# Performance work log

Measured on AMD Instinct MI355X. Metric: run time of the kernel, lower is better.

The kernel has to match this reference:

```python
import jax, jax.numpy as jnp
import numpy as np

D_MODEL = 1024
D_FF = 2048        # SwiGLU hidden (first linear outputs 2*D_FF)
NUM_EXPERTS = 8
TOP_K = 2
BATCH, SEQ = 2, 2048


def setup_inputs() -> dict:
    key = jax.random.key(0)
    ks = jax.random.split(key, 5)
    s = 0.02
    x = jax.random.normal(ks[0], (BATCH, SEQ, D_MODEL), jnp.float32)
    Wr = jax.random.normal(ks[1], (D_MODEL, NUM_EXPERTS), jnp.float32) * s
    temp = jnp.ones((1,), jnp.float32)  # router_temp parameter
    W1 = jax.random.normal(ks[2], (NUM_EXPERTS, D_MODEL, 2 * D_FF), jnp.float32) * s
    b1 = jnp.zeros((NUM_EXPERTS, 2 * D_FF), jnp.float32)
    W2 = jax.random.normal(ks[3], (NUM_EXPERTS, D_FF, D_MODEL), jnp.float32) * s
    b2 = jnp.zeros((NUM_EXPERTS, D_MODEL), jnp.float32)
    return {"x": x, "Wr": Wr, "temp": temp, "W1": W1, "b1": b1, "W2": W2, "b2": b2}


def reference(x, Wr, temp, W1, b1, W2, b2):
    # Eval-mode forward: no router noise, dropout is identity.
    B, S, D = x.shape
    xf = x.reshape(-1, D)                       # [T, D], T = B*S
    logits = (xf @ Wr) / temp                   # [T, E]
    topw, topi = jax.lax.top_k(logits, TOP_K)   # [T, K]
    topw = jax.nn.softmax(topw, axis=-1)        # renormalized top-k weights
    out = jnp.zeros_like(xf)
    for e in range(NUM_EXPERTS):                # small fixed expert count
        h = xf @ W1[e] + b1[e]                  # [T, 2F]
        a, g = jnp.split(h, 2, axis=-1)         # SwiGLU: a * silu(g)
        y = (a * jax.nn.silu(g)) @ W2[e] + b2[e]  # [T, D]
        # combine weight for expert e (0 if not routed to e)
        we = jnp.sum(jnp.where(topi == e, topw, 0.0), axis=-1, keepdims=True)
        out = out + y * we
    return out.reshape(B, S, D)
```

## Files before the change

kernel.cpp:

```cpp
#include <hip/hip_runtime.h>
#include <hip/hip_bf16.h>
#include <math.h>


#define T_TOK  4096
#define DMODEL 1024
#define NEXP   8
#define FF     2048
#define FF2    4096

typedef __bf16 bf16_t;
typedef bf16_t bf16x8 __attribute__((ext_vector_type(8)));
typedef float  f32x4  __attribute__((ext_vector_type(4)));

__device__ __forceinline__ void gload_lds16(const void* g, void* l) {
  __builtin_amdgcn_global_load_lds((const __attribute__((address_space(1))) void*)g,
                                   (__attribute__((address_space(3))) void*)l, 16, 0, 0);
}

__global__ __launch_bounds__(256) void moe_router(
    const float* __restrict__ x, const float* __restrict__ Wr,
    const float* __restrict__ temp,
    bf16_t* __restrict__ xb,
    int* __restrict__ cnt, int* __restrict__ tok_list, float* __restrict__ w_list,
    int* __restrict__ slot)
{
  __shared__ float sWr[DMODEL * NEXP];
  for (int i = threadIdx.x; i < DMODEL * NEXP; i += 256) sWr[i] = Wr[i];
  __syncthreads();

  int wave = threadIdx.x >> 6, lane = threadIdx.x & 63;
  int t = blockIdx.x * 4 + wave;
  const float* xr = x + (size_t)t * DMODEL;

  f32x4 acc0 = {0.f, 0.f, 0.f, 0.f}, acc1 = {0.f, 0.f, 0.f, 0.f};
  #pragma unroll
  for (int i = 0; i < 16; ++i) {
    int d = lane + 64 * i;
    float v = xr[d];
    xb[(size_t)t * DMODEL + d] = (bf16_t)v;
    const f32x4* wr = (const f32x4*)&sWr[d * NEXP];
    acc0 += v * wr[0];
    acc1 += v * wr[1];
  }
  #pragma unroll
  for (int off = 32; off; off >>= 1) {
    #pragma unroll
    for (int q = 0; q < 4; ++q) {
      acc0[q] += __shfl_down(acc0[q], off, 64);
      acc1[q] += __shfl_down(acc1[q], off, 64);
    }
  }
  if (lane == 0) {
    float invt = 1.f / temp[0];
    float lg[NEXP] = {acc0[0], acc0[1], acc0[2], acc0[3],
                      acc1[0], acc1[1], acc1[2], acc1[3]};
    int bi = 0, si = 0;
    float best = -3.4e38f, sec = -3.4e38f;
    #pragma unroll
    for (int e = 0; e < NEXP; ++e) {
      float l = lg[e] * invt;
      if (l > best)     { sec = best; si = bi; best = l; bi = e; }
      else if (l > sec) { sec = l; si = e; }
    }
    float ex = expf(sec - best);
    float wb  = 1.f / (1.f + ex);
    float wsc = ex  / (1.f + ex);
    int p0 = atomicAdd(&cnt[bi], 1);
    tok_list[bi * T_TOK + p0] = t; w_list[bi * T_TOK + p0] = wb;
    int p1 = atomicAdd(&cnt[si], 1);
    tok_list[si * T_TOK + p1] = t; w_list[si * T_TOK + p1] = wsc;
    slot[2 * t]     = bi * T_TOK + p0;
    slot[2 * t + 1] = si * T_TOK + p1;
  }
}

__global__ void moe_prefix(const int* __restrict__ cnt, int* __restrict__ offs) {
  if (threadIdx.x == 0) {
    int s = 0;
    for (int e = 0; e < NEXP; ++e) { offs[e] = s; s += cnt[e]; }
    offs[NEXP] = s;
  }
}

__global__ __launch_bounds__(256) void tcast_fast(
    const float* __restrict__ in, bf16_t* __restrict__ outp, int R, int C)
{
  __shared__ float tile[64][65];
  const float* inp = in + (size_t)blockIdx.z * R * C;
  bf16_t* op = outp + (size_t)blockIdx.z * R * C;
  int c0 = blockIdx.x * 64, r0 = blockIdx.y * 64;
  int tid = threadIdx.x;
  int lr = tid >> 4;
  int lc4 = (tid & 15) * 4;
  #pragma unroll
  for (int p = 0; p < 4; ++p) {
    int r = p * 16 + lr;
    const float4 v = *(const float4*)&inp[(size_t)(r0 + r) * C + c0 + lc4];
    tile[r][lc4 + 0] = v.x; tile[r][lc4 + 1] = v.y;
    tile[r][lc4 + 2] = v.z; tile[r][lc4 + 3] = v.w;
  }
  __syncthreads();
  int rr8 = (tid & 7) * 8;
  #pragma unroll
  for (int it = 0; it < 2; ++it) {
    int cc = (tid >> 3) + it * 32;
    bf16x8 o;
    #pragma unroll
    for (int j = 0; j < 8; ++j) o[j] = (bf16_t)tile[rr8 + j][cc];
    *(bf16x8*)&op[(size_t)(c0 + cc) * R + r0 + rr8] = o;
  }
}

__global__ __launch_bounds__(256) void moe_gemm1(
    const bf16_t* __restrict__ xb, const bf16_t* __restrict__ W1t,
    const float* __restrict__ b1, const int* __restrict__ cnt,
    const int* __restrict__ offs, const int* __restrict__ tok_list,
    const float* __restrict__ w_list, bf16_t* __restrict__ U,
    int e_base, long estride)
{
  int e = e_base + blockIdx.z;
  int count = cnt[e];
  int m0 = blockIdx.y * 128;
  if (m0 >= count) return;
  int nt = blockIdx.x;
  const bf16_t* W1e = W1t + (size_t)blockIdx.z * estride;

  __shared__ bf16_t As[128 * 64];
  __shared__ bf16_t Bs[128 * 64];
  __shared__ int   stok[128];
  __shared__ float sw[128];
  int tid = threadIdx.x;
  if (tid < 128) {
    int m = m0 + tid;
    stok[tid] = (m < count) ? tok_list[e * T_TOK + m] : 0;
    sw[tid]   = (m < count) ? w_list[e * T_TOK + m] : 0.f;
  }
  __syncthreads();

  int wave = tid >> 6, lane = tid & 63;
  int quad = lane >> 4, l16 = lane & 15;
  int rsub = lane >> 3;
  int swz  = (lane & 7) ^ rsub;

  size_t asrc[4]; const bf16_t* bsrc[4];
  bf16_t* aldst[4]; bf16_t* bldst[4];
  #pragma unroll
  for (int s = 0; s < 4; ++s) {
    int inst = wave * 4 + s;
    int row = inst * 8 + rsub;
    asrc[s] = (size_t)stok[row] * DMODEL + swz * 8;
    int grow = (row < 64) ? (nt * 64 + row) : (FF + nt * 64 + (row - 64));
    bsrc[s] = W1e + (size_t)grow * DMODEL + swz * 8;
    aldst[s] = As + inst * 512;
    bldst[s] = Bs + inst * 512;
  }

  f32x4 acc[2][8];
  #pragma unroll
  for (int i = 0; i < 2; ++i)
    #pragma unroll
    for (int j = 0; j < 8; ++j) acc[i][j] = (f32x4){0.f, 0.f, 0.f, 0.f};

  for (int k0 = 0; k0 < DMODEL; k0 += 64) {
    __syncthreads();
    #pragma unroll
    for (int s = 0; s < 4; ++s) {
      gload_lds16(xb + asrc[s] + k0, aldst[s]);
      gload_lds16(bsrc[s] + k0, bldst[s]);
    }
    __syncthreads();
    #pragma unroll
    for (int kh = 0; kh < 2; ++kh) {
      int so = ((kh * 4 + quad) ^ (l16 & 7)) * 8;
      bf16x8 a0 = *(const bf16x8*)&As[(wave * 32      + l16) * 64 + so];
      bf16x8 a1 = *(const bf16x8*)&As[(wave * 32 + 16 + l16) * 64 + so];
      #pragma unroll
      for (int j = 0; j < 8; ++j) {
        bf16x8 b = *(const bf16x8*)&Bs[(j * 16 + l16) * 64 + so];
        acc[0][j] = __builtin_amdgcn_mfma_f32_16x16x32_bf16(a0, b, acc[0][j], 0, 0, 0);
        acc[1][j] = __builtin_amdgcn_mfma_f32_16x16x32_bf16(a1, b, acc[1][j], 0, 0, 0);
      }
    }
  }

  int uoff = offs[e];
  const float* b1e = b1 + (size_t)e * FF2;
  #pragma unroll
  for (int j = 0; j < 4; ++j) {
    int f = nt * 64 + j * 16 + l16;
    float ba = b1e[f];
    float bg = b1e[FF + f];
    #pragma unroll
    for (int i = 0; i < 2; ++i) {
      f32x4 av = acc[i][j];
      f32x4 gv = acc[i][j + 4];
      #pragma unroll
      for (int r = 0; r < 4; ++r) {
        int m = wave * 32 + i * 16 + quad * 4 + r;
        if (m0 + m < count) {
          float aa = av[r] + ba;
          float gg = gv[r] + bg;
          float u = sw[m] * aa * gg / (1.f + __expf(-gg));
          U[(size_t)(uoff + m0 + m) * FF + f] = (bf16_t)u;
        }
      }
    }
  }
}

__global__ __launch_bounds__(256) void moe_gemm2(
    const bf16_t* __restrict__ U, const bf16_t* __restrict__ W2t,
    const int* __restrict__ cnt, const int* __restrict__ offs,
    float* __restrict__ Y,
    int e_base, long estride)
{
  int e = e_base + blockIdx.z;
  int count = cnt[e];
  int m0 = blockIdx.y * 128;
  if (m0 >= count) return;
  int n0 = blockIdx.x * 128;
  const bf16_t* W2e = W2t + (size_t)blockIdx.z * estride;

  __shared__ bf16_t As[128 * 64];
  __shared__ bf16_t Bs[128 * 64];
  int tid = threadIdx.x;
  int wave = tid >> 6, lane = tid & 63;
  int quad = lane >> 4, l16 = lane & 15;
  int rsub = lane >> 3;
  int swz  = (lane & 7) ^ rsub;
  int uoff = offs[e];

  const bf16_t* asrc[4]; const bf16_t* bsrc[4];
  bf16_t* aldst[4]; bf16_t* bldst[4];
  #pragma unroll
  for (int s = 0; s < 4; ++s) {
    int inst = wave * 4 + s;
    int row = inst * 8 + rsub;
    asrc[s] = U   + (size_t)(uoff + m0 + row) * FF + swz * 8;
    bsrc[s] = W2e + (size_t)(n0 + row)        * FF + swz * 8;
    aldst[s] = As + inst * 512;
    bldst[s] = Bs + inst * 512;
  }

  f32x4 acc[2][8];
  #pragma unroll
  for (int i = 0; i < 2; ++i)
    #pragma unroll
    for (int j = 0; j < 8; ++j) acc[i][j] = (f32x4){0.f, 0.f, 0.f, 0.f};

  for (int k0 = 0; k0 < FF; k0 += 64) {
    __syncthreads();
    #pragma unroll
    for (int s = 0; s < 4; ++s) {
      gload_lds16(asrc[s] + k0, aldst[s]);
      gload_lds16(bsrc[s] + k0, bldst[s]);
    }
    __syncthreads();
    #pragma unroll
    for (int kh = 0; kh < 2; ++kh) {
      int so = ((kh * 4 + quad) ^ (l16 & 7)) * 8;
      bf16x8 a0 = *(const bf16x8*)&As[(wave * 32      + l16) * 64 + so];
      bf16x8 a1 = *(const bf16x8*)&As[(wave * 32 + 16 + l16) * 64 + so];
      #pragma unroll
      for (int j = 0; j < 8; ++j) {
        bf16x8 b = *(const bf16x8*)&Bs[(j * 16 + l16) * 64 + so];
        acc[0][j] = __builtin_amdgcn_mfma_f32_16x16x32_bf16(a0, b, acc[0][j], 0, 0, 0);
        acc[1][j] = __builtin_amdgcn_mfma_f32_16x16x32_bf16(a1, b, acc[1][j], 0, 0, 0);
      }
    }
  }

  #pragma unroll
  for (int j = 0; j < 8; ++j) {
    int n = n0 + j * 16 + l16;
    #pragma unroll
    for (int i = 0; i < 2; ++i) {
      f32x4 av = acc[i][j];
      #pragma unroll
      for (int r = 0; r < 4; ++r) {
        int m = wave * 32 + i * 16 + quad * 4 + r;
        if (m0 + m < count)
          Y[(size_t)(uoff + m0 + m) * DMODEL + n] = av[r];
      }
    }
  }
}

__global__ __launch_bounds__(256) void moe_combine(
    const float* __restrict__ Y, const float* __restrict__ b2,
    const int* __restrict__ slot, const float* __restrict__ w_list,
    const int* __restrict__ offs, float* __restrict__ out)
{
  int t = blockIdx.x;
  int v0 = slot[2 * t], v1 = slot[2 * t + 1];
  int e0 = v0 >> 12, p0 = v0 & (T_TOK - 1);
  int e1 = v1 >> 12, p1 = v1 & (T_TOK - 1);
  int r0 = offs[e0] + p0, r1 = offs[e1] + p1;
  float w0 = w_list[v0], w1 = w_list[v1];
  int d = threadIdx.x * 4;
  f32x4 y0 = *(const f32x4*)&Y[(size_t)r0 * DMODEL + d];
  f32x4 y1 = *(const f32x4*)&Y[(size_t)r1 * DMODEL + d];
  f32x4 c0 = *(const f32x4*)&b2[(size_t)e0 * DMODEL + d];
  f32x4 c1 = *(const f32x4*)&b2[(size_t)e1 * DMODEL + d];
  *(f32x4*)&out[(size_t)t * DMODEL + d] = y0 + y1 + w0 * c0 + w1 * c1;
}

extern "C" void kernel_launch(void* const* d_in, const int* in_sizes, int n_in,
                              void* d_out, int out_size, void* d_ws, size_t ws_size,
                              hipStream_t stream)
{
  const float* x    = (const float*)d_in[0];
  const float* Wr   = (const float*)d_in[1];
  const float* temp = (const float*)d_in[2];
  const float* W1   = (const float*)d_in[3];
  const float* b1   = (const float*)d_in[4];
  const float* W2   = (const float*)d_in[5];
  const float* b2   = (const float*)d_in[6];
  float* out = (float*)d_out;

  char* ws = (char*)d_ws;
  size_t off = 0;
  auto alloc = [&](size_t b) { void* p = ws + off; off += (b + 255) & ~(size_t)255; return p; };
  bf16_t* xb  = (bf16_t*)alloc((size_t)T_TOK * DMODEL * 2);
  bf16_t* U   = (bf16_t*)alloc((size_t)(2 * T_TOK + 128) * FF * 2);
  float*  Y   = (float*)alloc((size_t)(2 * T_TOK) * DMODEL * 4);
  int*   cnt  = (int*)alloc(256);
  int*   offs = (int*)alloc(256);
  int*   tok  = (int*)alloc((size_t)NEXP * T_TOK * 4);
  float* wl   = (float*)alloc((size_t)NEXP * T_TOK * 4);
  int*   slot = (int*)alloc((size_t)2 * T_TOK * 4);
  size_t base = off;
  const size_t W1T_FULL = (size_t)NEXP * FF2 * DMODEL * 2;
  const size_t W2T_FULL = (size_t)NEXP * DMODEL * FF * 2;
  bool batched = (ws_size >= base + W1T_FULL + W2T_FULL);

  hipMemsetAsync(cnt, 0, NEXP * sizeof(int), stream);
  moe_router<<<dim3(T_TOK / 4), dim3(256), 0, stream>>>(x, Wr, temp, xb, cnt, tok, wl, slot);
  moe_prefix<<<dim3(1), dim3(64), 0, stream>>>(cnt, offs);

  if (batched) {
    bf16_t* W1t = (bf16_t*)alloc(W1T_FULL);
    bf16_t* W2t = (bf16_t*)alloc(W2T_FULL);
    tcast_fast<<<dim3(FF2 / 64, DMODEL / 64, NEXP), dim3(256), 0, stream>>>(W1, W1t, DMODEL, FF2);
    tcast_fast<<<dim3(DMODEL / 64, FF / 64, NEXP), dim3(256), 0, stream>>>(W2, W2t, FF, DMODEL);
    moe_gemm1<<<dim3(FF / 64, T_TOK / 128, NEXP), dim3(256), 0, stream>>>(
        xb, W1t, b1, cnt, offs, tok, wl, U, 0, (long)FF2 * DMODEL);
    moe_gemm2<<<dim3(DMODEL / 128, T_TOK / 128, NEXP), dim3(256), 0, stream>>>(
        U, W2t, cnt, offs, Y, 0, (long)DMODEL * FF);
  } else {
    bf16_t* W1t = (bf16_t*)alloc((size_t)FF2 * DMODEL * 2);
    bf16_t* W2t = (bf16_t*)alloc((size_t)DMODEL * FF * 2);
    for (int e = 0; e < NEXP; ++e) {
      tcast_fast<<<dim3(FF2 / 64, DMODEL / 64, 1), dim3(256), 0, stream>>>(
          W1 + (size_t)e * DMODEL * FF2, W1t, DMODEL, FF2);
      moe_gemm1<<<dim3(FF / 64, T_TOK / 128, 1), dim3(256), 0, stream>>>(
          xb, W1t, b1, cnt, offs, tok, wl, U, e, 0);
    }
    for (int e = 0; e < NEXP; ++e) {
      tcast_fast<<<dim3(DMODEL / 64, FF / 64, 1), dim3(256), 0, stream>>>(
          W2 + (size_t)e * FF * DMODEL, W2t, FF, DMODEL);
      moe_gemm2<<<dim3(DMODEL / 128, T_TOK / 128, 1), dim3(256), 0, stream>>>(
          U, W2t, cnt, offs, Y, e, 0);
    }
  }
  moe_combine<<<dim3(T_TOK), dim3(256), 0, stream>>>(Y, b2, slot, wl, offs, out);
}
```

Before: 536.5 us.

## Rewrite gemm1 as 256x256 double-buffered pipelined tile with 8 waves

The first expert GEMM moves from a 128x128 single-buffered tile with 4 waves to a 256x(128 up + 128 gate) tile with 8 waves and 2 blocks per CU. LDS is double-buffered, and global-to-LDS loads for the next K step are interleaved between four MFMA phases, with s_setprio raised around the MFMA bursts. The aim is to hide load latency behind compute and raise arithmetic intensity per LDS byte. In exchange it uses far more LDS and registers, and padding waste grows for experts whose token counts are not multiples of 256.

```diff
diff --git a/kernel.cpp b/kernel.cpp
--- a/kernel.cpp
+++ b/kernel.cpp
@@ -8,6 +8,7 @@
 #define NEXP   8
 #define FF     2048
 #define FF2    4096
+#define NT1    16
 
 typedef __bf16 bf16_t;
 typedef bf16_t bf16x8 __attribute__((ext_vector_type(8)));
@@ -17,6 +18,10 @@
   __builtin_amdgcn_global_load_lds((const __attribute__((address_space(1))) void*)g,
                                    (__attribute__((address_space(3))) void*)l, 16, 0, 0);
 }
+
+#define BARF() do { asm volatile("" ::: "memory"); \
+                    __builtin_amdgcn_s_barrier();  \
+                    asm volatile("" ::: "memory"); } while (0)
 
 __global__ __launch_bounds__(256) void moe_router(
     const float* __restrict__ x, const float* __restrict__ Wr,
@@ -112,7 +117,18 @@
   }
 }
 
-__global__ __launch_bounds__(256) void moe_gemm1(
+#define STG_A1(buf, ha, kk) do { \
+    gload_lds16(xb + asrc[ha][0] + (kk), &As[buf][aofs[ha][0]]); \
+    gload_lds16(xb + asrc[ha][1] + (kk), &As[buf][aofs[ha][1]]); } while (0)
+#define STG_B1(buf, hb, kk) do { \
+    gload_lds16(W1e + bsrc[hb][0] + (kk), &Bs[buf][bofs[hb][0]]); \
+    gload_lds16(W1e + bsrc[hb][1] + (kk), &Bs[buf][bofs[hb][1]]); } while (0)
+#define LDA1(dst, rowbase, kh_) \
+    dst = *(const bf16x8*)&As[cur][((rowbase) + l16) * 64 + ((((kh_) * 4 + quad) ^ (l16 & 7)) * 8)]
+#define LDB1(dst, rowbase, kh_) \
+    dst = *(const bf16x8*)&Bs[cur][((rowbase) + l16) * 64 + ((((kh_) * 4 + quad) ^ (l16 & 7)) * 8)]
+
+__global__ __launch_bounds__(512, 2) void moe_gemm1(
     const bf16_t* __restrict__ xb, const bf16_t* __restrict__ W1t,
     const float* __restrict__ b1, const int* __restrict__ cnt,
     const int* __restrict__ offs, const int* __restrict__ tok_list,
@@ -121,92 +137,152 @@
 {
   int e = e_base + blockIdx.z;
   int count = cnt[e];
-  int m0 = blockIdx.y * 128;
+  int m0 = blockIdx.y * 256;
   if (m0 >= count) return;
   int nt = blockIdx.x;
   const bf16_t* W1e = W1t + (size_t)blockIdx.z * estride;
 
-  __shared__ bf16_t As[128 * 64];
-  __shared__ bf16_t Bs[128 * 64];
-  __shared__ int   stok[128];
-  __shared__ float sw[128];
+  __shared__ bf16_t As[2][256 * 64];
+  __shared__ bf16_t Bs[2][256 * 64];
+
   int tid = threadIdx.x;
-  if (tid < 128) {
-    int m = m0 + tid;
-    stok[tid] = (m < count) ? tok_list[e * T_TOK + m] : 0;
-    sw[tid]   = (m < count) ? w_list[e * T_TOK + m] : 0.f;
-  }
-  __syncthreads();
-
-  int wave = tid >> 6, lane = tid & 63;
+  int w = tid >> 6, lane = tid & 63;
+  int wm = w >> 2, wn = w & 3;
   int quad = lane >> 4, l16 = lane & 15;
-  int rsub = lane >> 3;
-  int swz  = (lane & 7) ^ rsub;
-
-  size_t asrc[4]; const bf16_t* bsrc[4];
-  bf16_t* aldst[4]; bf16_t* bldst[4];
-  #pragma unroll
-  for (int s = 0; s < 4; ++s) {
-    int inst = wave * 4 + s;
-    int row = inst * 8 + rsub;
-    asrc[s] = (size_t)stok[row] * DMODEL + swz * 8;
-    int grow = (row < 64) ? (nt * 64 + row) : (FF + nt * 64 + (row - 64));
-    bsrc[s] = W1e + (size_t)grow * DMODEL + swz * 8;
-    aldst[s] = As + inst * 512;
-    bldst[s] = Bs + inst * 512;
-  }
-
-  f32x4 acc[2][8];
-  #pragma unroll
-  for (int i = 0; i < 2; ++i)
-    #pragma unroll
-    for (int j = 0; j < 8; ++j) acc[i][j] = (f32x4){0.f, 0.f, 0.f, 0.f};
-
-  for (int k0 = 0; k0 < DMODEL; k0 += 64) {
-    __syncthreads();
-    #pragma unroll
-    for (int s = 0; s < 4; ++s) {
-      gload_lds16(xb + asrc[s] + k0, aldst[s]);
-      gload_lds16(bsrc[s] + k0, bldst[s]);
-    }
-    __syncthreads();
-    #pragma unroll
-    for (int kh = 0; kh < 2; ++kh) {
-      int so = ((kh * 4 + quad) ^ (l16 & 7)) * 8;
-      bf16x8 a0 = *(const bf16x8*)&As[(wave * 32      + l16) * 64 + so];
-      bf16x8 a1 = *(const bf16x8*)&As[(wave * 32 + 16 + l16) * 64 + so];
-      #pragma unroll
-      for (int j = 0; j < 8; ++j) {
-        bf16x8 b = *(const bf16x8*)&Bs[(j * 16 + l16) * 64 + so];
-        acc[0][j] = __builtin_amdgcn_mfma_f32_16x16x32_bf16(a0, b, acc[0][j], 0, 0, 0);
-        acc[1][j] = __builtin_amdgcn_mfma_f32_16x16x32_bf16(a1, b, acc[1][j], 0, 0, 0);
-      }
-    }
+  int rsub = lane >> 3, csub = lane & 7;
+  int swz = csub ^ rsub;
+
+  unsigned asrc[2][2], bsrc[2][2];
+  int aofs[2][2], bofs[2][2];
+  #pragma unroll
+  for (int h = 0; h < 2; ++h) {
+    #pragma unroll
+    for (int i = 0; i < 2; ++i) {
+      int rb = h * 128 + w * 16 + i * 8;
+      int r = rb + rsub;
+      int gm = m0 + r;
+      int tokr = (gm < count) ? tok_list[e * T_TOK + gm] : 0;
+      asrc[h][i] = (unsigned)tokr * DMODEL + swz * 8;
+      aofs[h][i] = rb * 64;
+      int wn_r = r >> 6, j = r & 63;
+      int f = nt * 128 + wn_r * 32 + (j & 31);
+      bsrc[h][i] = (unsigned)((j < 32) ? f : (FF + f)) * DMODEL + swz * 8;
+      bofs[h][i] = rb * 64;
+    }
+  }
+
+  f32x4 acc[8][4];
+  #pragma unroll
+  for (int m = 0; m < 8; ++m)
+    #pragma unroll
+    for (int n = 0; n < 4; ++n) acc[m][n] = (f32x4){0.f, 0.f, 0.f, 0.f};
+  bf16x8 a0[4][2], a1[4][2], bb[2][2];
+
+  STG_A1(0, 0, 0); STG_A1(0, 1, 0);
+  STG_B1(0, 0, 0); STG_B1(0, 1, 0);
+  STG_A1(1, 0, 64); STG_A1(1, 1, 64);
+  asm volatile("s_waitcnt vmcnt(4)" ::: "memory");
+  BARF();
+
+  for (int t = 0; t < NT1; ++t) {
+    const int cur = t & 1, nxt = cur ^ 1;
+    const int k1 = ((t + 1 < NT1) ? t + 1 : NT1 - 1) * 64;
+    const int k2 = ((t + 2 < NT1) ? t + 2 : NT1 - 1) * 64;
+
+    STG_B1(nxt, 0, k1);
+    #pragma unroll
+    for (int m = 0; m < 4; ++m)
+      #pragma unroll
+      for (int kh = 0; kh < 2; ++kh) LDA1(a0[m][kh], wm * 128 + m * 16, kh);
+    #pragma unroll
+    for (int n = 0; n < 2; ++n)
+      #pragma unroll
+      for (int kh = 0; kh < 2; ++kh) LDB1(bb[n][kh], wn * 64 + n * 16, kh);
+    BARF();
+    __builtin_amdgcn_s_setprio(1);
+    #pragma unroll
+    for (int m = 0; m < 4; ++m)
+      #pragma unroll
+      for (int n = 0; n < 2; ++n)
+        #pragma unroll
+        for (int kh = 0; kh < 2; ++kh)
+          acc[m][n] = __builtin_amdgcn_mfma_f32_16x16x32_bf16(a0[m][kh], bb[n][kh], acc[m][n], 0, 0, 0);
+    __builtin_amdgcn_s_setprio(0);
+    BARF();
+
+    STG_B1(nxt, 1, k1);
+    #pragma unroll
+    for (int m = 0; m < 4; ++m)
+      #pragma unroll
+      for (int kh = 0; kh < 2; ++kh) LDA1(a1[m][kh], wm * 128 + 64 + m * 16, kh);
+    BARF();
+    __builtin_amdgcn_s_setprio(1);
+    #pragma unroll
+    for (int m = 0; m < 4; ++m)
+      #pragma unroll
+      for (int n = 0; n < 2; ++n)
+        #pragma unroll
+        for (int kh = 0; kh < 2; ++kh)
+          acc[4 + m][n] = __builtin_amdgcn_mfma_f32_16x16x32_bf16(a1[m][kh], bb[n][kh], acc[4 + m][n], 0, 0, 0);
+    __builtin_amdgcn_s_setprio(0);
+    BARF();
+
+    STG_A1(cur, 0, k2);
+    #pragma unroll
+    for (int n = 0; n < 2; ++n)
+      #pragma unroll
+      for (int kh = 0; kh < 2; ++kh) LDB1(bb[n][kh], wn * 64 + (2 + n) * 16, kh);
+    BARF();
+    __builtin_amdgcn_s_setprio(1);
+    #pragma unroll
+    for (int m = 0; m < 4; ++m)
+      #pragma unroll
+      for (int n = 0; n < 2; ++n)
+        #pragma unroll
+        for (int kh = 0; kh < 2; ++kh)
+          acc[m][2 + n] = __builtin_amdgcn_mfma_f32_16x16x32_bf16(a0[m][kh], bb[n][kh], acc[m][2 + n], 0, 0, 0);
+    __builtin_amdgcn_s_setprio(0);
+    BARF();
+
+    STG_A1(cur, 1, k2);
+    __builtin_amdgcn_s_setprio(1);
+    #pragma unroll
+    for (int m = 0; m < 4; ++m)
+      #pragma unroll
+      for (int n = 0; n < 2; ++n)
+        #pragma unroll
+        for (int kh = 0; kh < 2; ++kh)
+          acc[4 + m][2 + n] = __builtin_amdgcn_mfma_f32_16x16x32_bf16(a1[m][kh], bb[n][kh], acc[4 + m][2 + n], 0, 0, 0);
+    __builtin_amdgcn_s_setprio(0);
+    asm volatile("s_waitcnt vmcnt(4)" ::: "memory");
+    BARF();
   }
 
   int uoff = offs[e];
   const float* b1e = b1 + (size_t)e * FF2;
   #pragma unroll
-  for (int j = 0; j < 4; ++j) {
-    int f = nt * 64 + j * 16 + l16;
+  for (int nf = 0; nf < 2; ++nf) {
+    int f = nt * 128 + wn * 32 + nf * 16 + l16;
     float ba = b1e[f];
     float bg = b1e[FF + f];
     #pragma unroll
-    for (int i = 0; i < 2; ++i) {
-      f32x4 av = acc[i][j];
-      f32x4 gv = acc[i][j + 4];
+    for (int m = 0; m < 8; ++m) {
+      f32x4 av = acc[m][nf];
+      f32x4 gv = acc[m][2 + nf];
       #pragma unroll
       for (int r = 0; r < 4; ++r) {
-        int m = wave * 32 + i * 16 + quad * 4 + r;
-        if (m0 + m < count) {
+        int row = wm * 128 + m * 16 + quad * 4 + r;
+        if (m0 + row < count) {
+          float wv = w_list[e * T_TOK + m0 + row];
           float aa = av[r] + ba;
           float gg = gv[r] + bg;
-          float u = sw[m] * aa * gg / (1.f + __expf(-gg));
-          U[(size_t)(uoff + m0 + m) * FF + f] = (bf16_t)u;
+          float u = wv * aa * gg / (1.f + __expf(-gg));
+          U[(size_t)(uoff + m0 + row) * FF + f] = (bf16_t)u;
         }
       }
     }
   }
+  asm volatile("s_waitcnt vmcnt(0)" ::: "memory");
 }
 
 __global__ __launch_bounds__(256) void moe_gemm2(
@@ -344,7 +420,7 @@
     bf16_t* W2t = (bf16_t*)alloc(W2T_FULL);
     tcast_fast<<<dim3(FF2 / 64, DMODEL / 64, NEXP), dim3(256), 0, stream>>>(W1, W1t, DMODEL, FF2);
     tcast_fast<<<dim3(DMODEL / 64, FF / 64, NEXP), dim3(256), 0, stream>>>(W2, W2t, FF, DMODEL);
-    moe_gemm1<<<dim3(FF / 64, T_TOK / 128, NEXP), dim3(256), 0, stream>>>(
+    moe_gemm1<<<dim3(FF / 128, T_TOK / 256, NEXP), dim3(512), 0, stream>>>(
         xb, W1t, b1, cnt, offs, tok, wl, U, 0, (long)FF2 * DMODEL);
     moe_gemm2<<<dim3(DMODEL / 128, T_TOK / 128, NEXP), dim3(256), 0, stream>>>(
         U, W2t, cnt, offs, Y, 0, (long)DMODEL * FF);
@@ -354,7 +430,7 @@
     for (int e = 0; e < NEXP; ++e) {
       tcast_fast<<<dim3(FF2 / 64, DMODEL / 64, 1), dim3(256), 0, stream>>>(
           W1 + (size_t)e * DMODEL * FF2, W1t, DMODEL, FF2);
-      moe_gemm1<<<dim3(FF / 64, T_TOK / 128, 1), dim3(256), 0, stream>>>(
+      moe_gemm1<<<dim3(FF / 128, T_TOK / 256, 1), dim3(512), 0, stream>>>(
           xb, W1t, b1, cnt, offs, tok, wl, U, e, 0);
     }
     for (int e = 0; e < NEXP; ++e) {
```

Result: slower. 571.3 us (+6.5%).
